# Performance work log

Measured on AMD Instinct MI355X. Metric: run time of the kernel, lower is better.

The kernel has to match this reference:

```python
import jax, jax.numpy as jnp
import numpy as np
import math

B, A, T = 64, 23, 128          # batch, num_agents, max seq len
D, AE, S, H = 256, 32, 6, 8    # d_model, agent_encoding_dim, static_dim, heads
DK = D // H                     # 32
DM = D + AE                     # 288, MHA q/k/v dim
NEG = -1e10                     # masked_fill constant from source


def sinusoidal_pe(pos, d):
    # pos: int array [...], returns [..., d] standard transformer PE at positions pos
    half = jnp.arange(d // 2, dtype=jnp.float32)
    div = jnp.exp(-half * (math.log(10000.0) * 2.0 / d))          # [d/2]
    ang = pos[..., None].astype(jnp.float32) * div                # [..., d/2]
    return jnp.stack([jnp.sin(ang), jnp.cos(ang)], axis=-1).reshape(*pos.shape, d)


def setup_inputs() -> dict:
    key = jax.random.key(0)
    ks = jax.random.split(key, 20)
    std = 0.02
    data = jax.random.normal(ks[0], (B, A, T), jnp.float32)
    lengths = jax.random.randint(ks[1], (B, A), 0, T + 1).astype(jnp.int32)   # mask arg = lengths
    t = jnp.arange(T, dtype=jnp.int32)
    time = jnp.where(t[None, None, :] < lengths[:, :, None], t[None, None, :], -1)  # [B,A,T], -1 = pad
    static = jax.random.normal(ks[2], (B, S), jnp.float32)
    # per-agent Linear(1, D): weight [A, D], bias [A, D]
    W_embed = std * jax.random.normal(ks[3], (A, D), jnp.float32)
    b_embed = std * jax.random.normal(ks[4], (A, D), jnp.float32)
    E_var = std * jax.random.normal(ks[5], (A, AE), jnp.float32)            # VariateEncoding table
    W_static = std * jax.random.normal(ks[6], (S, D), jnp.float32)
    b_static = jnp.zeros((D,), jnp.float32)
    Wq = std * jax.random.normal(ks[7], (DM, D), jnp.float32); bq = jnp.zeros((D,), jnp.float32)
    Wk = std * jax.random.normal(ks[8], (DM, D), jnp.float32); bk = jnp.zeros((D,), jnp.float32)
    Wv = std * jax.random.normal(ks[9], (DM, D), jnp.float32); bv = jnp.zeros((D,), jnp.float32)
    Wo = std * jax.random.normal(ks[10], (D, DM), jnp.float32); bo = jnp.zeros((DM,), jnp.float32)
    Wg = std * jax.random.normal(ks[11], (DM + D, 1), jnp.float32); bg = jnp.zeros((1,), jnp.float32)
    return dict(data=data, time=time, mask=lengths, static=static,
                W_embed=W_embed, b_embed=b_embed, E_var=E_var,
                W_static=W_static, b_static=b_static,
                Wq=Wq, bq=bq, Wk=Wk, bk=bk, Wv=Wv, bv=bv, Wo=Wo, bo=bo,
                Wg=Wg, bg=bg)


def reference(data, time, mask, static, W_embed, b_embed, E_var, W_static, b_static,
              Wq, bq, Wk, bk, Wv, bv, Wo, bo, Wg, bg):
    lengths = mask                                            # [B,A] sequence lengths
    t = jnp.arange(T)
    valid = t[None, None, :] < lengths[:, :, None]            # [B,A,T] bool
    # mask_matrix[i,:len,:len]=1 double loop -> vectorized outer product
    mask4 = valid[:, :, :, None] & valid[:, :, None, :]       # [B,A,T,T]

    # per-agent Linear(1, D) loop -> batched rank-1 affine, then ReLU
    data_embeds = jax.nn.relu(data[..., None] * W_embed[None, :, None, :]
                              + b_embed[None, :, None, :])    # [B,A,T,D]

    # src_pe: sinusoidal positional encoding at (clamped) time values
    pe = sinusoidal_pe(jnp.maximum(time, 0), D)               # [B,A,T,D]
    src = data_embeds + pe

    # variate (agent-id) embedding concat -> [B,A,T,D+AE]; encoder = identity
    var = jnp.broadcast_to(E_var[None, :, None, :], (B, A, T, AE))
    memory = jnp.concatenate([src, var], axis=-1)             # [B,A,T,DM]

    # time-masked mean pool over T
    time_mask = time >= 0                                     # [B,A,T]
    memory = jnp.where(time_mask[..., None], memory, 0.0)
    counts = time_mask.sum(axis=2).astype(memory.dtype)       # [B,A]
    agentwise = memory.sum(axis=2) / (counts[..., None] + 1e-9)  # [B,A,DM]

    # custom MHA (dim='Time'): q_len = 1 per agent, keys/values over T
    q = jnp.einsum('bae,ed->bad', agentwise, Wq) + bq          # [B,A,D]
    k = jnp.einsum('bate,ed->batd', memory, Wk) + bk           # [B,A,T,D]
    v = jnp.einsum('bate,ed->batd', memory, Wv) + bv
    qh = q.reshape(B, A, H, DK)                                # [B,A,H,DK] (q_len=1 squeezed)
    kh = k.reshape(B, A, T, H, DK).transpose(0, 1, 3, 2, 4)    # [B,A,H,T,DK]
    vh = v.reshape(B, A, T, H, DK).transpose(0, 1, 3, 2, 4)
    scores = jnp.einsum('bahd,bahtd->baht', qh, kh) / math.sqrt(DK)  # [B,A,H,T]
    amask = mask4[:, :, 0, :]                                  # [B,A,T] row 0 of per-agent mask
    scores = jnp.where(amask[:, :, None, :], scores, NEG)
    p = jax.nn.softmax(scores, axis=-1)                        # dropout = eval (identity)
    ctx = jnp.einsum('baht,bahtd->bahd', p, vh).reshape(B, A, D)
    agent_feat = jnp.einsum('bad,de->bae', ctx, Wo) + bo       # [B,A,DM]

    # agent-masked mean pool over agents
    agent_mask = counts > 0                                    # [B,A]
    agent_feat = jnp.where(agent_mask[..., None], agent_feat, 0.0)
    denom = agent_mask.sum(axis=1).astype(agent_feat.dtype) + 1e-9
    aggre = agent_feat.sum(axis=1) / denom[:, None]            # [B,DM]

    static_feat = static @ W_static + b_static                 # [B,D]
    all_feature = jnp.concatenate([aggre, static_feat], axis=-1)  # [B,DM+D]
    return all_feature @ Wg + bg                               # [B,1]


if __name__ == '__main__':
    out = reference(**setup_inputs())
    print(out.shape, jnp.asarray(out).dtype)
```

## Files before the change

### kernel.cpp

```cpp
#include <hip/hip_runtime.h>
#include <math.h>

#define NB 64
#define NA 23
#define NT 128
#define ND 256
#define NAE 32
#define NS 6
#define NH 8
#define NDM 288

#define OFF_PET    0
#define OFF_PECUM  32768
#define OFF_WKT    65792
#define OFF_VWO    131328
#define OFF_CST    133632
#define OFF_S      133648

__global__ __launch_bounds__(256) void setup_kernel(
    const float* __restrict__ Wk, const float* __restrict__ Wv,
    const float* __restrict__ Wo, const float* __restrict__ Wg,
    const float* __restrict__ bv, const float* __restrict__ bo,
    const float* __restrict__ W_static, const float* __restrict__ b_static,
    const float* __restrict__ bg, float* __restrict__ ws)
{
    const int blk = blockIdx.x;
    const int tid = threadIdx.x;
    float* peT   = ws + OFF_PET;
    float* PEcum = ws + OFF_PECUM;
    float* WkT   = ws + OFF_WKT;
    float* VWo   = ws + OFF_VWO;
    float* cst   = ws + OFF_CST;

    if (blk < 128) {
        const int g = tid >> 7, t = tid & 127;
        const int e = blk * 2 + g;
        const int i = e >> 1;
        const float kdiv = 0.07195578415606394f;
        const float dv = expf(-(float)i * kdiv);
        const float ang = (float)t * dv;
        const float v = (e & 1) ? cosf(ang) : sinf(ang);
        peT[e * NT + t] = v;
        __shared__ float buf[256];
        buf[tid] = v;
        #pragma unroll
        for (int s = 1; s < 128; s <<= 1) {
            __syncthreads();
            float add = (t >= s) ? buf[tid - s] : 0.f;
            __syncthreads();
            buf[tid] += add;
        }
        __syncthreads();
        PEcum[(t + 1) * ND + e] = buf[tid];
    } else if (blk < 384) {
        const int j = blk - 128;
        const float scale = 0.17677669529663687f;
        WkT[j * 256 + tid] = Wk[tid * ND + j] * scale;
    } else if (blk < 392) {
        const int h = blk - 384;
        __shared__ float wog[32];
        {
            const int jj = tid >> 3, sub = tid & 7;
            const int j = h * 32 + jj;
            float acc = 0.f;
            const int m0 = sub * 36;
            #pragma unroll 4
            for (int m = m0; m < m0 + 36; ++m)
                acc = fmaf(Wo[j * NDM + m], Wg[m], acc);
            acc += __shfl_down(acc, 4, 8);
            acc += __shfl_down(acc, 2, 8);
            acc += __shfl_down(acc, 1, 8);
            if (sub == 0) wog[jj] = acc;
        }
        __syncthreads();
        for (int e = tid; e < NDM; e += 256) {
            float acc = 0.f;
            #pragma unroll 8
            for (int jj = 0; jj < 32; ++jj)
                acc = fmaf(Wv[e * ND + h * 32 + jj], wog[jj], acc);
            VWo[h * NDM + e] = acc;
        }
        if (tid == 0) {
            float acc = 0.f;
            #pragma unroll 8
            for (int jj = 0; jj < 32; ++jj)
                acc = fmaf(bv[h * 32 + jj], wog[jj], acc);
            cst[8 + h] = acc;
        }
    } else {
        const int i = tid >> 5, sub = tid & 31;
        float acc = 0.f;
        if (i < 6) {
            for (int m = sub; m < 256; m += 32)
                acc = fmaf(W_static[i * ND + m], Wg[NDM + m], acc);
        } else if (i == 6) {
            for (int m = sub; m < 256; m += 32)
                acc = fmaf(b_static[m], Wg[NDM + m], acc);
        } else {
            for (int m = sub; m < NDM; m += 32)
                acc = fmaf(bo[m], Wg[m], acc);
        }
        #pragma unroll
        for (int off = 16; off > 0; off >>= 1)
            acc += __shfl_down(acc, off, 32);
        if (sub == 0) cst[i] = (i == 6) ? acc + bg[0] : acc;
    }
}

__global__ __launch_bounds__(256) void main_kernel(
    const float* __restrict__ data, const int* __restrict__ lengths,
    const float* __restrict__ W_embed, const float* __restrict__ b_embed,
    const float* __restrict__ E_var,
    const float* __restrict__ Wq, const float* __restrict__ bq,
    float* __restrict__ ws)
{
    const int wg = blockIdx.x;
    const int a = wg % NA;
    const int tid = threadIdx.x;
    const int L = lengths[wg];

    if (L == 0) {
        if (tid == 0) ws[OFF_S + wg] = 0.f;
        return;
    }

    __shared__ float xs[NT];
    __shared__ float agentwise[NDM];
    __shared__ float qs[ND];
    __shared__ float2 Wb[ND];
    __shared__ __align__(16) float combo[ND * 16];
    __shared__ float evvS[NH];
    __shared__ float red[4];

    const float* peT   = ws + OFF_PET;
    const float* PEcum = ws + OFF_PECUM;
    const float* WkT   = ws + OFF_WKT;
    const float* VWo   = ws + OFF_VWO;
    const float* cstp  = ws + OFF_CST;

    if (tid < NT) xs[tid] = data[wg * NT + tid];
    __syncthreads();
    {
        const int e = tid;
        const float We = W_embed[a * ND + e];
        const float be = b_embed[a * ND + e];
        Wb[e] = make_float2(We, be);
        float acc = 0.f;
        #pragma unroll 4
        for (int t = 0; t < L; ++t)
            acc += fmaxf(fmaf(xs[t], We, be), 0.f);
        agentwise[e] = (acc + PEcum[L * ND + e]) / (float)L;
    }
    if (tid < NAE) agentwise[ND + tid] = E_var[a * NAE + tid];
    __syncthreads();

    {
        const int j = tid;
        float acc = bq[j];
        #pragma unroll 4
        for (int f = 0; f < NDM; ++f)
            acc = fmaf(agentwise[f], Wq[f * ND + j], acc);
        qs[j] = acc;
    }
    __syncthreads();

    {
        const int h = tid >> 5, eo = tid & 31;
        const float* wr = WkT + (h * 32) * 256;
        for (int eb = 0; eb < 8; ++eb) {
            const int e = eb * 32 + eo;
            float acc = 0.f;
            #pragma unroll 8
            for (int j = 0; j < 32; ++j)
                acc = fmaf(wr[j * 256 + e], qs[h * 32 + j], acc);
            combo[e * 16 + h] = acc;
        }
    }
    for (int idx = tid; idx < NH * ND; idx += 256) {
        const int h = idx >> 8, e = idx & 255;
        combo[e * 16 + 8 + h] = VWo[h * NDM + e];
    }
    {
        const int h = tid >> 5, ee = tid & 31;
        float v = E_var[a * NAE + ee] * VWo[h * NDM + ND + ee];
        v += __shfl_down(v, 16, 32);
        v += __shfl_down(v, 8, 32);
        v += __shfl_down(v, 4, 32);
        v += __shfl_down(v, 2, 32);
        v += __shfl_down(v, 1, 32);
        if (ee == 0) evvS[h] = v;
    }
    __syncthreads();

    {
        const int t = tid & 127;
        const int half = tid >> 7;
        const float xt = xs[t];
        float accS[8], accM[8];
        #pragma unroll
        for (int h = 0; h < 8; ++h) { accS[h] = 0.f; accM[h] = 0.f; }
        const int ebase = half * 128;
        const float4* comboV = (const float4*)combo + ebase * 4;
        const float* peCol = peT + ebase * NT + t;
        #pragma unroll 2
        for (int ee = 0; ee < 128; ++ee) {
            const float2 wb = Wb[ebase + ee];
            const float m = fmaxf(fmaf(xt, wb.x, wb.y), 0.f) + peCol[ee * NT];
            const float4 c0 = comboV[ee * 4 + 0];
            const float4 c1 = comboV[ee * 4 + 1];
            const float4 c2 = comboV[ee * 4 + 2];
            const float4 c3 = comboV[ee * 4 + 3];
            accS[0] = fmaf(m, c0.x, accS[0]);
            accS[1] = fmaf(m, c0.y, accS[1]);
            accS[2] = fmaf(m, c0.z, accS[2]);
            accS[3] = fmaf(m, c0.w, accS[3]);
            accS[4] = fmaf(m, c1.x, accS[4]);
            accS[5] = fmaf(m, c1.y, accS[5]);
            accS[6] = fmaf(m, c1.z, accS[6]);
            accS[7] = fmaf(m, c1.w, accS[7]);
            accM[0] = fmaf(m, c2.x, accM[0]);
            accM[1] = fmaf(m, c2.y, accM[1]);
            accM[2] = fmaf(m, c2.z, accM[2]);
            accM[3] = fmaf(m, c2.w, accM[3]);
            accM[4] = fmaf(m, c3.x, accM[4]);
            accM[5] = fmaf(m, c3.y, accM[5]);
            accM[6] = fmaf(m, c3.z, accM[6]);
            accM[7] = fmaf(m, c3.w, accM[7]);
        }
        __syncthreads();
        float* sc   = combo;
        float* mvb  = combo + 1024;
        float* scP1 = combo + 2048;
        float* mvP1 = combo + 3072;
        if (half == 1) {
            #pragma unroll
            for (int h = 0; h < 8; ++h) {
                scP1[h * NT + t] = accS[h];
                mvP1[h * NT + t] = accM[h];
            }
        }
        __syncthreads();
        if (half == 0) {
            #pragma unroll
            for (int h = 0; h < 8; ++h) {
                sc[h * NT + t]  = accS[h] + scP1[h * NT + t];
                mvb[h * NT + t] = accM[h] + mvP1[h * NT + t];
            }
        }
    }
    __syncthreads();

    {
        const float* sc  = combo;
        const float* mvb = combo + 1024;
        const int wv = tid >> 6, lane = tid & 63;
        float wsum = 0.f;
        for (int hh = 0; hh < 2; ++hh) {
            const int h = wv * 2 + hh;
            float s1 = (lane < L) ? sc[h * NT + lane] : -3e38f;
            float s2 = (lane + 64 < L) ? sc[h * NT + 64 + lane] : -3e38f;
            float mx = fmaxf(s1, s2);
            #pragma unroll
            for (int off = 32; off > 0; off >>= 1)
                mx = fmaxf(mx, __shfl_down(mx, off, 64));
            mx = __shfl(mx, 0, 64);
            const float vbv = evvS[h] + cstp[8 + h];
            float e1 = (lane < L) ? __expf(s1 - mx) : 0.f;
            float e2 = (lane + 64 < L) ? __expf(s2 - mx) : 0.f;
            float num = e1 * (mvb[h * NT + lane] + vbv);
            num = fmaf(e2, mvb[h * NT + 64 + lane] + vbv, num);
            float den = e1 + e2;
            #pragma unroll
            for (int off = 32; off > 0; off >>= 1) {
                num += __shfl_down(num, off, 64);
                den += __shfl_down(den, off, 64);
            }
            if (lane == 0) wsum += num / den;
        }
        if (lane == 0) red[wv] = wsum;
    }
    __syncthreads();
    if (tid == 0) {
        ws[OFF_S + wg] = cstp[7] + red[0] + red[1] + red[2] + red[3];
    }
}

__global__ __launch_bounds__(64) void final_kernel(
    const float* __restrict__ statics, const int* __restrict__ lengths,
    const float* __restrict__ ws, float* __restrict__ out)
{
    const int b = threadIdx.x;
    const float* s_arr = ws + OFF_S;
    const float* cst = ws + OFF_CST;
    float sum = 0.f;
    int n = 0;
    for (int a = 0; a < NA; ++a) {
        if (lengths[b * NA + a] > 0) { sum += s_arr[b * NA + a]; ++n; }
    }
    float o = sum / ((float)n + 1e-9f);
    #pragma unroll
    for (int i = 0; i < NS; ++i)
        o = fmaf(statics[b * NS + i], cst[i], o);
    o += cst[6];
    out[b] = o;
}

extern "C" void kernel_launch(void* const* d_in, const int* in_sizes, int n_in,
                              void* d_out, int out_size, void* d_ws, size_t ws_size,
                              hipStream_t stream) {
    const float* data     = (const float*)d_in[0];
    const int*   mask     = (const int*)d_in[2];
    const float* statics  = (const float*)d_in[3];
    const float* W_embed  = (const float*)d_in[4];
    const float* b_embed  = (const float*)d_in[5];
    const float* E_var    = (const float*)d_in[6];
    const float* W_static = (const float*)d_in[7];
    const float* b_static = (const float*)d_in[8];
    const float* Wq       = (const float*)d_in[9];
    const float* bq       = (const float*)d_in[10];
    const float* Wk       = (const float*)d_in[11];
    const float* Wv       = (const float*)d_in[13];
    const float* bv       = (const float*)d_in[14];
    const float* Wo       = (const float*)d_in[15];
    const float* bo       = (const float*)d_in[16];
    const float* Wg       = (const float*)d_in[17];
    const float* bg       = (const float*)d_in[18];
    float* out = (float*)d_out;
    float* ws  = (float*)d_ws;

    setup_kernel<<<dim3(393), dim3(256), 0, stream>>>(Wk, Wv, Wo, Wg, bv, bo,
                                                      W_static, b_static, bg, ws);
    main_kernel<<<dim3(NB * NA), dim3(256), 0, stream>>>(data, mask, W_embed, b_embed,
                                                         E_var, Wq, bq, ws);
    final_kernel<<<dim3(1), dim3(64), 0, stream>>>(statics, mask, ws, out);
}
```

Baseline: 165.5 us.

## Fuse final reduction into main kernel and adapt score loop to sequence length

Removes the separate final kernel: each block bumps a global atomic counter, and the last block to finish computes the per-batch masked mean and static projection. The main kernel also vectorises the Q projection with float4 Wq loads split over four chunks, uses multiple accumulators in the embedding-sum and K-fold loops, and pads the combo layout to a stride of 20. For sequences of length 64 or less, the score/value loop splits the embedding dimension four ways instead of two, which halves per-thread work. The counter is reset inside the setup kernel, and the fused tail adds atomics and fences in exchange for one fewer launch.

Measured after the change: 214.6 us. 29.7% more time.

```diff
diff --git a/kernel.cpp b/kernel.cpp
--- a/kernel.cpp
+++ b/kernel.cpp
@@ -12,6 +12,7 @@
 
 #define OFF_PET    0
 #define OFF_PECUM  32768
+#define OFF_CNT    32768
 #define OFF_WKT    65792
 #define OFF_VWO    131328
 #define OFF_CST    133632
@@ -88,6 +89,7 @@
             cst[8 + h] = acc;
         }
     } else {
+        if (tid == 0) ws[OFF_CNT] = 0.0f;
         const int i = tid >> 5, sub = tid & 31;
         float acc = 0.f;
         if (i < 6) {
@@ -112,6 +114,7 @@
     const float* __restrict__ W_embed, const float* __restrict__ b_embed,
     const float* __restrict__ E_var,
     const float* __restrict__ Wq, const float* __restrict__ bq,
+    const float* __restrict__ statics, float* __restrict__ out,
     float* __restrict__ ws)
 {
     const int wg = blockIdx.x;
@@ -119,18 +122,14 @@
     const int tid = threadIdx.x;
     const int L = lengths[wg];
 
-    if (L == 0) {
-        if (tid == 0) ws[OFF_S + wg] = 0.f;
-        return;
-    }
-
     __shared__ float xs[NT];
     __shared__ float agentwise[NDM];
     __shared__ float qs[ND];
     __shared__ float2 Wb[ND];
-    __shared__ __align__(16) float combo[ND * 16];
+    __shared__ __align__(16) float combo[ND * 20];
     __shared__ float evvS[NH];
     __shared__ float red[4];
+    __shared__ int lastFlag;
 
     const float* peT   = ws + OFF_PET;
     const float* PEcum = ws + OFF_PECUM;
@@ -138,171 +137,211 @@
     const float* VWo   = ws + OFF_VWO;
     const float* cstp  = ws + OFF_CST;
 
-    if (tid < NT) xs[tid] = data[wg * NT + tid];
-    __syncthreads();
-    {
-        const int e = tid;
-        const float We = W_embed[a * ND + e];
-        const float be = b_embed[a * ND + e];
-        Wb[e] = make_float2(We, be);
-        float acc = 0.f;
-        #pragma unroll 4
-        for (int t = 0; t < L; ++t)
-            acc += fmaxf(fmaf(xs[t], We, be), 0.f);
-        agentwise[e] = (acc + PEcum[L * ND + e]) / (float)L;
+    if (L > 0) {
+        if (tid < NT) xs[tid] = data[wg * NT + tid];
+        __syncthreads();
+        {
+            const int e = tid;
+            const float We = W_embed[a * ND + e];
+            const float be = b_embed[a * ND + e];
+            Wb[e] = make_float2(We, be);
+            float s0 = 0.f, s1 = 0.f, s2 = 0.f, s3 = 0.f;
+            int t = 0;
+            for (; t + 4 <= L; t += 4) {
+                s0 += fmaxf(fmaf(xs[t],     We, be), 0.f);
+                s1 += fmaxf(fmaf(xs[t + 1], We, be), 0.f);
+                s2 += fmaxf(fmaf(xs[t + 2], We, be), 0.f);
+                s3 += fmaxf(fmaf(xs[t + 3], We, be), 0.f);
+            }
+            for (; t < L; ++t)
+                s0 += fmaxf(fmaf(xs[t], We, be), 0.f);
+            agentwise[e] = (((s0 + s1) + (s2 + s3)) + PEcum[L * ND + e]) / (float)L;
+        }
+        if (tid < NAE) agentwise[ND + tid] = E_var[a * NAE + tid];
+        __syncthreads();
+
+        {
+            const int lane = tid & 63;
+            const int fc = tid >> 6;
+            const float4* Wq4 = (const float4*)Wq;
+            float a0 = 0.f, a1 = 0.f, a2 = 0.f, a3 = 0.f;
+            const int f0 = fc * 72;
+            #pragma unroll 4
+            for (int f = f0; f < f0 + 72; ++f) {
+                const float ag = agentwise[f];
+                const float4 w = Wq4[f * 64 + lane];
+                a0 = fmaf(ag, w.x, a0);
+                a1 = fmaf(ag, w.y, a1);
+                a2 = fmaf(ag, w.z, a2);
+                a3 = fmaf(ag, w.w, a3);
+            }
+            ((float4*)combo)[fc * 64 + lane] = make_float4(a0, a1, a2, a3);
+        }
+        __syncthreads();
+        qs[tid] = bq[tid] + combo[tid] + combo[256 + tid] + combo[512 + tid] + combo[768 + tid];
+        __syncthreads();
+
+        {
+            const int h = tid >> 5, eo = tid & 31;
+            const float* wr = WkT + (h * 32) * 256;
+            const float* qh = qs + h * 32;
+            for (int eb = 0; eb < 8; ++eb) {
+                const int e = eb * 32 + eo;
+                float acc = 0.f, acc2 = 0.f;
+                #pragma unroll
+                for (int j = 0; j < 32; j += 2) {
+                    acc  = fmaf(wr[ j      * 256 + e], qh[j],     acc);
+                    acc2 = fmaf(wr[(j + 1) * 256 + e], qh[j + 1], acc2);
+                }
+                combo[e * 20 + h] = acc + acc2;
+            }
+        }
+        for (int idx = tid; idx < NH * ND; idx += 256) {
+            const int h = idx >> 8, e = idx & 255;
+            combo[e * 20 + 8 + h] = VWo[h * NDM + e];
+        }
+        {
+            const int h = tid >> 5, ee = tid & 31;
+            float v = agentwise[ND + ee] * VWo[h * NDM + ND + ee];
+            v += __shfl_down(v, 16, 32);
+            v += __shfl_down(v, 8, 32);
+            v += __shfl_down(v, 4, 32);
+            v += __shfl_down(v, 2, 32);
+            v += __shfl_down(v, 1, 32);
+            if (ee == 0) evvS[h] = v;
+        }
+        __syncthreads();
+
+        {
+            const int shift = (L > 64) ? 7 : 6;
+            const int Tpad  = 1 << shift;
+            const int P     = 256 >> shift;
+            const int t     = tid & (Tpad - 1);
+            const int c     = tid >> shift;
+            const int ebase = c * Tpad;
+            const float xt = xs[t];
+            float accS[8], accM[8];
+            #pragma unroll
+            for (int h = 0; h < 8; ++h) { accS[h] = 0.f; accM[h] = 0.f; }
+            const float4* comboV = (const float4*)combo;
+            const float* peCol = peT + ebase * NT + t;
+            #pragma unroll 2
+            for (int ee = 0; ee < Tpad; ++ee) {
+                const int e = ebase + ee;
+                const float2 wb = Wb[e];
+                const float m = fmaxf(fmaf(xt, wb.x, wb.y), 0.f) + peCol[ee * NT];
+                const float4 c0 = comboV[e * 5 + 0];
+                const float4 c1 = comboV[e * 5 + 1];
+                const float4 c2 = comboV[e * 5 + 2];
+                const float4 c3 = comboV[e * 5 + 3];
+                accS[0] = fmaf(m, c0.x, accS[0]);
+                accS[1] = fmaf(m, c0.y, accS[1]);
+                accS[2] = fmaf(m, c0.z, accS[2]);
+                accS[3] = fmaf(m, c0.w, accS[3]);
+                accS[4] = fmaf(m, c1.x, accS[4]);
+                accS[5] = fmaf(m, c1.y, accS[5]);
+                accS[6] = fmaf(m, c1.z, accS[6]);
+                accS[7] = fmaf(m, c1.w, accS[7]);
+                accM[0] = fmaf(m, c2.x, accM[0]);
+                accM[1] = fmaf(m, c2.y, accM[1]);
+                accM[2] = fmaf(m, c2.z, accM[2]);
+                accM[3] = fmaf(m, c2.w, accM[3]);
+                accM[4] = fmaf(m, c3.x, accM[4]);
+                accM[5] = fmaf(m, c3.y, accM[5]);
+                accM[6] = fmaf(m, c3.z, accM[6]);
+                accM[7] = fmaf(m, c3.w, accM[7]);
+            }
+            __syncthreads();
+            float* sc  = combo;
+            float* mvb = combo + 1024;
+            float* sp  = combo + 2048;
+            float* mp  = sp + (P - 1) * 8 * Tpad;
+            if (c > 0) {
+                float* spc = sp + (c - 1) * 8 * Tpad;
+                float* mpc = mp + (c - 1) * 8 * Tpad;
+                #pragma unroll
+                for (int h = 0; h < 8; ++h) {
+                    spc[h * Tpad + t] = accS[h];
+                    mpc[h * Tpad + t] = accM[h];
+                }
+            }
+            __syncthreads();
+            if (c == 0) {
+                #pragma unroll
+                for (int h = 0; h < 8; ++h) {
+                    float s = accS[h], m = accM[h];
+                    for (int cc = 0; cc < P - 1; ++cc) {
+                        s += sp[cc * 8 * Tpad + h * Tpad + t];
+                        m += mp[cc * 8 * Tpad + h * Tpad + t];
+                    }
+                    sc[h * NT + t]  = s;
+                    mvb[h * NT + t] = m;
+                }
+            }
+        }
+        __syncthreads();
+
+        {
+            const float* sc  = combo;
+            const float* mvb = combo + 1024;
+            const int wv = tid >> 6, lane = tid & 63;
+            float wsum = 0.f;
+            for (int hh = 0; hh < 2; ++hh) {
+                const int h = wv * 2 + hh;
+                float s1 = (lane < L) ? sc[h * NT + lane] : -3e38f;
+                float s2 = (lane + 64 < L) ? sc[h * NT + 64 + lane] : -3e38f;
+                float mx = fmaxf(s1, s2);
+                #pragma unroll
+                for (int off = 32; off > 0; off >>= 1)
+                    mx = fmaxf(mx, __shfl_down(mx, off, 64));
+                mx = __shfl(mx, 0, 64);
+                const float vbv = evvS[h] + cstp[8 + h];
+                float e1 = (lane < L) ? __expf(s1 - mx) : 0.f;
+                float e2 = (lane + 64 < L) ? __expf(s2 - mx) : 0.f;
+                float num = e1 * (mvb[h * NT + lane] + vbv);
+                num = fmaf(e2, mvb[h * NT + 64 + lane] + vbv, num);
+                float den = e1 + e2;
+                #pragma unroll
+                for (int off = 32; off > 0; off >>= 1) {
+                    num += __shfl_down(num, off, 64);
+                    den += __shfl_down(den, off, 64);
+                }
+                if (lane == 0) wsum += num / den;
+            }
+            if (lane == 0) red[wv] = wsum;
+        }
+        __syncthreads();
+        if (tid == 0)
+            ws[OFF_S + wg] = cstp[7] + red[0] + red[1] + red[2] + red[3];
+    } else {
+        if (tid == 0) ws[OFF_S + wg] = 0.f;
     }
-    if (tid < NAE) agentwise[ND + tid] = E_var[a * NAE + tid];
-    __syncthreads();
-
-    {
-        const int j = tid;
-        float acc = bq[j];
-        #pragma unroll 4
-        for (int f = 0; f < NDM; ++f)
-            acc = fmaf(agentwise[f], Wq[f * ND + j], acc);
-        qs[j] = acc;
+
+    if (tid == 0) {
+        __threadfence();
+        const int prev = atomicAdd((int*)(ws + OFF_CNT), 1);
+        lastFlag = (prev == NB * NA - 1) ? 1 : 0;
     }
     __syncthreads();
-
-    {
-        const int h = tid >> 5, eo = tid & 31;
-        const float* wr = WkT + (h * 32) * 256;
-        for (int eb = 0; eb < 8; ++eb) {
-            const int e = eb * 32 + eo;
-            float acc = 0.f;
-            #pragma unroll 8
-            for (int j = 0; j < 32; ++j)
-                acc = fmaf(wr[j * 256 + e], qs[h * 32 + j], acc);
-            combo[e * 16 + h] = acc;
-        }
+    if (lastFlag && tid < NB) {
+        __threadfence();
+        const int b = tid;
+        float* s_arr = ws + OFF_S;
+        float sum = 0.f;
+        int n = 0;
+        for (int aa = 0; aa < NA; ++aa) {
+            if (lengths[b * NA + aa] > 0) {
+                sum += atomicAdd(s_arr + b * NA + aa, 0.f);
+                ++n;
+            }
+        }
+        float o = sum / ((float)n + 1e-9f);
+        #pragma unroll
+        for (int i = 0; i < NS; ++i)
+            o = fmaf(statics[b * NS + i], cstp[i], o);
+        o += cstp[6];
+        out[b] = o;
     }
-    for (int idx = tid; idx < NH * ND; idx += 256) {
-        const int h = idx >> 8, e = idx & 255;
-        combo[e * 16 + 8 + h] = VWo[h * NDM + e];
-    }
-    {
-        const int h = tid >> 5, ee = tid & 31;
-        float v = E_var[a * NAE + ee] * VWo[h * NDM + ND + ee];
-        v += __shfl_down(v, 16, 32);
-        v += __shfl_down(v, 8, 32);
-        v += __shfl_down(v, 4, 32);
-        v += __shfl_down(v, 2, 32);
-        v += __shfl_down(v, 1, 32);
-        if (ee == 0) evvS[h] = v;
-    }
-    __syncthreads();
-
-    {
-        const int t = tid & 127;
-        const int half = tid >> 7;
-        const float xt = xs[t];
-        float accS[8], accM[8];
-        #pragma unroll
-        for (int h = 0; h < 8; ++h) { accS[h] = 0.f; accM[h] = 0.f; }
-        const int ebase = half * 128;
-        const float4* comboV = (const float4*)combo + ebase * 4;
-        const float* peCol = peT + ebase * NT + t;
-        #pragma unroll 2
-        for (int ee = 0; ee < 128; ++ee) {
-            const float2 wb = Wb[ebase + ee];
-            const float m = fmaxf(fmaf(xt, wb.x, wb.y), 0.f) + peCol[ee * NT];
-            const float4 c0 = comboV[ee * 4 + 0];
-            const float4 c1 = comboV[ee * 4 + 1];
-            const float4 c2 = comboV[ee * 4 + 2];
-            const float4 c3 = comboV[ee * 4 + 3];
-            accS[0] = fmaf(m, c0.x, accS[0]);
-            accS[1] = fmaf(m, c0.y, accS[1]);
-            accS[2] = fmaf(m, c0.z, accS[2]);
-            accS[3] = fmaf(m, c0.w, accS[3]);
-            accS[4] = fmaf(m, c1.x, accS[4]);
-            accS[5] = fmaf(m, c1.y, accS[5]);
-            accS[6] = fmaf(m, c1.z, accS[6]);
-            accS[7] = fmaf(m, c1.w, accS[7]);
-            accM[0] = fmaf(m, c2.x, accM[0]);
-            accM[1] = fmaf(m, c2.y, accM[1]);
-            accM[2] = fmaf(m, c2.z, accM[2]);
-            accM[3] = fmaf(m, c2.w, accM[3]);
-            accM[4] = fmaf(m, c3.x, accM[4]);
-            accM[5] = fmaf(m, c3.y, accM[5]);
-            accM[6] = fmaf(m, c3.z, accM[6]);
-            accM[7] = fmaf(m, c3.w, accM[7]);
-        }
-        __syncthreads();
-        float* sc   = combo;
-        float* mvb  = combo + 1024;
-        float* scP1 = combo + 2048;
-        float* mvP1 = combo + 3072;
-        if (half == 1) {
-            #pragma unroll
-            for (int h = 0; h < 8; ++h) {
-                scP1[h * NT + t] = accS[h];
-                mvP1[h * NT + t] = accM[h];
-            }
-        }
-        __syncthreads();
-        if (half == 0) {
-            #pragma unroll
-            for (int h = 0; h < 8; ++h) {
-                sc[h * NT + t]  = accS[h] + scP1[h * NT + t];
-                mvb[h * NT + t] = accM[h] + mvP1[h * NT + t];
-            }
-        }
-    }
-    __syncthreads();
-
-    {
-        const float* sc  = combo;
-        const float* mvb = combo + 1024;
-        const int wv = tid >> 6, lane = tid & 63;
-        float wsum = 0.f;
-        for (int hh = 0; hh < 2; ++hh) {
-            const int h = wv * 2 + hh;
-            float s1 = (lane < L) ? sc[h * NT + lane] : -3e38f;
-            float s2 = (lane + 64 < L) ? sc[h * NT + 64 + lane] : -3e38f;
-            float mx = fmaxf(s1, s2);
-            #pragma unroll
-            for (int off = 32; off > 0; off >>= 1)
-                mx = fmaxf(mx, __shfl_down(mx, off, 64));
-            mx = __shfl(mx, 0, 64);
-            const float vbv = evvS[h] + cstp[8 + h];
-            float e1 = (lane < L) ? __expf(s1 - mx) : 0.f;
-            float e2 = (lane + 64 < L) ? __expf(s2 - mx) : 0.f;
-            float num = e1 * (mvb[h * NT + lane] + vbv);
-            num = fmaf(e2, mvb[h * NT + 64 + lane] + vbv, num);
-            float den = e1 + e2;
-            #pragma unroll
-            for (int off = 32; off > 0; off >>= 1) {
-                num += __shfl_down(num, off, 64);
-                den += __shfl_down(den, off, 64);
-            }
-            if (lane == 0) wsum += num / den;
-        }
-        if (lane == 0) red[wv] = wsum;
-    }
-    __syncthreads();
-    if (tid == 0) {
-        ws[OFF_S + wg] = cstp[7] + red[0] + red[1] + red[2] + red[3];
-    }
-}
-
-__global__ __launch_bounds__(64) void final_kernel(
-    const float* __restrict__ statics, const int* __restrict__ lengths,
-    const float* __restrict__ ws, float* __restrict__ out)
-{
-    const int b = threadIdx.x;
-    const float* s_arr = ws + OFF_S;
-    const float* cst = ws + OFF_CST;
-    float sum = 0.f;
-    int n = 0;
-    for (int a = 0; a < NA; ++a) {
-        if (lengths[b * NA + a] > 0) { sum += s_arr[b * NA + a]; ++n; }
-    }
-    float o = sum / ((float)n + 1e-9f);
-    #pragma unroll
-    for (int i = 0; i < NS; ++i)
-        o = fmaf(statics[b * NS + i], cst[i], o);
-    o += cst[6];
-    out[b] = o;
 }
 
 extern "C" void kernel_launch(void* const* d_in, const int* in_sizes, int n_in,
@@ -331,6 +370,5 @@
     setup_kernel<<<dim3(393), dim3(256), 0, stream>>>(Wk, Wv, Wo, Wg, bv, bo,
                                                       W_static, b_static, bg, ws);
     main_kernel<<<dim3(NB * NA), dim3(256), 0, stream>>>(data, mask, W_embed, b_embed,
-                                                         E_var, Wq, bq, ws);
-    final_kernel<<<dim3(1), dim3(64), 0, stream>>>(statics, mask, ws, out);
+                                                         E_var, Wq, bq, statics, out, ws);
 }
```

## Restructure main kernel projections, swizzle combo layout, add short-sequence path

Applied to the files above, without the earlier changes.

The setup kernel now copies Wk scaled in its original layout with float4 loads instead of transposing it. In the main kernel, the q projection is split across four waves that each read float4 Wq rows, with the partial sums combined through shared memory. The K-fold becomes a per-thread dot product over contiguous Wk rows, and combo rows are XOR-swizzled to cut LDS bank conflicts. The embedding and PE inner loop gets multiple accumulators and PE prefetching, and a separate path for L<=64 splits the feature dimension four ways so that no threads sit idle on padded timesteps. The cost is more code, extra shared-memory reductions and a larger register footprint.

New measurement: 192.4 us. 1.16x slower.

```diff
diff --git a/kernel.cpp b/kernel.cpp
--- a/kernel.cpp
+++ b/kernel.cpp
@@ -12,7 +12,7 @@
 
 #define OFF_PET    0
 #define OFF_PECUM  32768
-#define OFF_WKT    65792
+#define OFF_WKS    65792
 #define OFF_VWO    131328
 #define OFF_CST    133632
 #define OFF_S      133648
@@ -28,7 +28,6 @@
     const int tid = threadIdx.x;
     float* peT   = ws + OFF_PET;
     float* PEcum = ws + OFF_PECUM;
-    float* WkT   = ws + OFF_WKT;
     float* VWo   = ws + OFF_VWO;
     float* cst   = ws + OFF_CST;
 
@@ -52,12 +51,14 @@
         }
         __syncthreads();
         PEcum[(t + 1) * ND + e] = buf[tid];
-    } else if (blk < 384) {
-        const int j = blk - 128;
+    } else if (blk < 192) {
         const float scale = 0.17677669529663687f;
-        WkT[j * 256 + tid] = Wk[tid * ND + j] * scale;
-    } else if (blk < 392) {
-        const int h = blk - 384;
+        const int i = (blk - 128) * 256 + tid;
+        const float4 w = ((const float4*)Wk)[i];
+        ((float4*)(ws + OFF_WKS))[i] = make_float4(w.x * scale, w.y * scale,
+                                                   w.z * scale, w.w * scale);
+    } else if (blk < 200) {
+        const int h = blk - 192;
         __shared__ float wog[32];
         {
             const int jj = tid >> 3, sub = tid & 7;
@@ -107,6 +108,38 @@
     }
 }
 
+#define EBODY(EE, RR) do {                                                   \
+    const int e_ = ebase + (EE);                                             \
+    const float2 wb = Wb[e_];                                                \
+    const float m = fmaxf(fmaf(xt, wb.x, wb.y), 0.f) + pcur[RR];             \
+    const float4 c0 = comboV[e_ * 4 + (0 ^ (RR))];                           \
+    const float4 c1 = comboV[e_ * 4 + (1 ^ (RR))];                           \
+    const float4 c2 = comboV[e_ * 4 + (2 ^ (RR))];                           \
+    const float4 c3 = comboV[e_ * 4 + (3 ^ (RR))];                           \
+    accS[0] = fmaf(m, c0.x, accS[0]); accS[1] = fmaf(m, c0.y, accS[1]);      \
+    accS[2] = fmaf(m, c0.z, accS[2]); accS[3] = fmaf(m, c0.w, accS[3]);      \
+    accS[4] = fmaf(m, c1.x, accS[4]); accS[5] = fmaf(m, c1.y, accS[5]);      \
+    accS[6] = fmaf(m, c1.z, accS[6]); accS[7] = fmaf(m, c1.w, accS[7]);      \
+    accM[0] = fmaf(m, c2.x, accM[0]); accM[1] = fmaf(m, c2.y, accM[1]);      \
+    accM[2] = fmaf(m, c2.z, accM[2]); accM[3] = fmaf(m, c2.w, accM[3]);      \
+    accM[4] = fmaf(m, c3.x, accM[4]); accM[5] = fmaf(m, c3.y, accM[5]);      \
+    accM[6] = fmaf(m, c3.z, accM[6]); accM[7] = fmaf(m, c3.w, accM[7]);      \
+} while (0)
+
+#define E_LOOP(TPC)                                                          \
+    pcur[0] = peCol[0 * NT]; pcur[1] = peCol[1 * NT];                        \
+    pcur[2] = peCol[2 * NT]; pcur[3] = peCol[3 * NT];                        \
+    _Pragma("unroll 2")                                                      \
+    for (int ee = 0; ee < (TPC); ee += 4) {                                  \
+        const float pn0 = peCol[(ee + 4) * NT];                              \
+        const float pn1 = peCol[(ee + 5) * NT];                              \
+        const float pn2 = peCol[(ee + 6) * NT];                              \
+        const float pn3 = peCol[(ee + 7) * NT];                              \
+        EBODY(ee + 0, 0); EBODY(ee + 1, 1);                                  \
+        EBODY(ee + 2, 2); EBODY(ee + 3, 3);                                  \
+        pcur[0] = pn0; pcur[1] = pn1; pcur[2] = pn2; pcur[3] = pn3;          \
+    }
+
 __global__ __launch_bounds__(256) void main_kernel(
     const float* __restrict__ data, const int* __restrict__ lengths,
     const float* __restrict__ W_embed, const float* __restrict__ b_embed,
@@ -126,7 +159,7 @@
 
     __shared__ float xs[NT];
     __shared__ float agentwise[NDM];
-    __shared__ float qs[ND];
+    __shared__ __align__(16) float qs[ND];
     __shared__ float2 Wb[ND];
     __shared__ __align__(16) float combo[ND * 16];
     __shared__ float evvS[NH];
@@ -134,7 +167,7 @@
 
     const float* peT   = ws + OFF_PET;
     const float* PEcum = ws + OFF_PECUM;
-    const float* WkT   = ws + OFF_WKT;
+    const float* WkS   = ws + OFF_WKS;
     const float* VWo   = ws + OFF_VWO;
     const float* cstp  = ws + OFF_CST;
 
@@ -145,44 +178,74 @@
         const float We = W_embed[a * ND + e];
         const float be = b_embed[a * ND + e];
         Wb[e] = make_float2(We, be);
-        float acc = 0.f;
+        float s0 = 0.f, s1 = 0.f, s2 = 0.f, s3 = 0.f;
+        int t = 0;
+        for (; t + 4 <= L; t += 4) {
+            s0 += fmaxf(fmaf(xs[t],     We, be), 0.f);
+            s1 += fmaxf(fmaf(xs[t + 1], We, be), 0.f);
+            s2 += fmaxf(fmaf(xs[t + 2], We, be), 0.f);
+            s3 += fmaxf(fmaf(xs[t + 3], We, be), 0.f);
+        }
+        for (; t < L; ++t)
+            s0 += fmaxf(fmaf(xs[t], We, be), 0.f);
+        agentwise[e] = (((s0 + s1) + (s2 + s3)) + PEcum[L * ND + e]) / (float)L;
+    }
+    if (tid < NAE) agentwise[ND + tid] = E_var[a * NAE + tid];
+    __syncthreads();
+
+    {
+        const int lane = tid & 63;
+        const int fc = tid >> 6;
+        const float4* Wq4 = (const float4*)Wq;
+        float a0 = 0.f, a1 = 0.f, a2 = 0.f, a3 = 0.f;
+        const int f0 = fc * 72;
         #pragma unroll 4
-        for (int t = 0; t < L; ++t)
-            acc += fmaxf(fmaf(xs[t], We, be), 0.f);
-        agentwise[e] = (acc + PEcum[L * ND + e]) / (float)L;
-    }
-    if (tid < NAE) agentwise[ND + tid] = E_var[a * NAE + tid];
+        for (int f = f0; f < f0 + 72; ++f) {
+            const float ag = agentwise[f];
+            const float4 w = Wq4[f * 64 + lane];
+            a0 = fmaf(ag, w.x, a0);
+            a1 = fmaf(ag, w.y, a1);
+            a2 = fmaf(ag, w.z, a2);
+            a3 = fmaf(ag, w.w, a3);
+        }
+        ((float4*)combo)[fc * 64 + lane] = make_float4(a0, a1, a2, a3);
+    }
+    __syncthreads();
+    qs[tid] = bq[tid] + combo[tid] + combo[256 + tid] + combo[512 + tid] + combo[768 + tid];
     __syncthreads();
 
     {
-        const int j = tid;
-        float acc = bq[j];
-        #pragma unroll 4
-        for (int f = 0; f < NDM; ++f)
-            acc = fmaf(agentwise[f], Wq[f * ND + j], acc);
-        qs[j] = acc;
-    }
-    __syncthreads();
-
-    {
-        const int h = tid >> 5, eo = tid & 31;
-        const float* wr = WkT + (h * 32) * 256;
-        for (int eb = 0; eb < 8; ++eb) {
-            const int e = eb * 32 + eo;
-            float acc = 0.f;
-            #pragma unroll 8
-            for (int j = 0; j < 32; ++j)
-                acc = fmaf(wr[j * 256 + e], qs[h * 32 + j], acc);
-            combo[e * 16 + h] = acc;
-        }
-    }
-    for (int idx = tid; idx < NH * ND; idx += 256) {
-        const int h = idx >> 8, e = idx & 255;
-        combo[e * 16 + 8 + h] = VWo[h * NDM + e];
+        const int e = tid;
+        const float4* wrow = (const float4*)(WkS + e * 256);
+        const float4* qs4  = (const float4*)qs;
+        float qk[8];
+        #pragma unroll
+        for (int h = 0; h < 8; ++h) {
+            float a0 = 0.f, a1 = 0.f, a2 = 0.f, a3 = 0.f;
+            #pragma unroll
+            for (int jq = 0; jq < 8; ++jq) {
+                const float4 w = wrow[h * 8 + jq];
+                const float4 q = qs4[h * 8 + jq];
+                a0 = fmaf(w.x, q.x, a0);
+                a1 = fmaf(w.y, q.y, a1);
+                a2 = fmaf(w.z, q.z, a2);
+                a3 = fmaf(w.w, q.w, a3);
+            }
+            qk[h] = (a0 + a1) + (a2 + a3);
+        }
+        float vwo[8];
+        #pragma unroll
+        for (int h = 0; h < 8; ++h) vwo[h] = VWo[h * NDM + e];
+        const int r = e & 3;
+        float4* row = (float4*)combo + e * 4;
+        row[0 ^ r] = make_float4(qk[0], qk[1], qk[2], qk[3]);
+        row[1 ^ r] = make_float4(qk[4], qk[5], qk[6], qk[7]);
+        row[2 ^ r] = make_float4(vwo[0], vwo[1], vwo[2], vwo[3]);
+        row[3 ^ r] = make_float4(vwo[4], vwo[5], vwo[6], vwo[7]);
     }
     {
         const int h = tid >> 5, ee = tid & 31;
-        float v = E_var[a * NAE + ee] * VWo[h * NDM + ND + ee];
+        float v = agentwise[ND + ee] * VWo[h * NDM + ND + ee];
         v += __shfl_down(v, 16, 32);
         v += __shfl_down(v, 8, 32);
         v += __shfl_down(v, 4, 32);
@@ -192,41 +255,17 @@
     }
     __syncthreads();
 
-    {
-        const int t = tid & 127;
-        const int half = tid >> 7;
+    const float4* comboV = (const float4*)combo;
+    if (L > 64) {
+        const int t = tid & 127, half = tid >> 7;
+        const int ebase = half * 128;
         const float xt = xs[t];
+        const float* peCol = peT + ebase * NT + t;
+        float pcur[4];
         float accS[8], accM[8];
         #pragma unroll
         for (int h = 0; h < 8; ++h) { accS[h] = 0.f; accM[h] = 0.f; }
-        const int ebase = half * 128;
-        const float4* comboV = (const float4*)combo + ebase * 4;
-        const float* peCol = peT + ebase * NT + t;
-        #pragma unroll 2
-        for (int ee = 0; ee < 128; ++ee) {
-            const float2 wb = Wb[ebase + ee];
-            const float m = fmaxf(fmaf(xt, wb.x, wb.y), 0.f) + peCol[ee * NT];
-            const float4 c0 = comboV[ee * 4 + 0];
-            const float4 c1 = comboV[ee * 4 + 1];
-            const float4 c2 = comboV[ee * 4 + 2];
-            const float4 c3 = comboV[ee * 4 + 3];
-            accS[0] = fmaf(m, c0.x, accS[0]);
-            accS[1] = fmaf(m, c0.y, accS[1]);
-            accS[2] = fmaf(m, c0.z, accS[2]);
-            accS[3] = fmaf(m, c0.w, accS[3]);
-            accS[4] = fmaf(m, c1.x, accS[4]);
-            accS[5] = fmaf(m, c1.y, accS[5]);
-            accS[6] = fmaf(m, c1.z, accS[6]);
-            accS[7] = fmaf(m, c1.w, accS[7]);
-            accM[0] = fmaf(m, c2.x, accM[0]);
-            accM[1] = fmaf(m, c2.y, accM[1]);
-            accM[2] = fmaf(m, c2.z, accM[2]);
-            accM[3] = fmaf(m, c2.w, accM[3]);
-            accM[4] = fmaf(m, c3.x, accM[4]);
-            accM[5] = fmaf(m, c3.y, accM[5]);
-            accM[6] = fmaf(m, c3.z, accM[6]);
-            accM[7] = fmaf(m, c3.w, accM[7]);
-        }
+        E_LOOP(128);
         __syncthreads();
         float* sc   = combo;
         float* mvb  = combo + 1024;
@@ -247,42 +286,97 @@
                 mvb[h * NT + t] = accM[h] + mvP1[h * NT + t];
             }
         }
-    }
-    __syncthreads();
-
-    {
-        const float* sc  = combo;
-        const float* mvb = combo + 1024;
-        const int wv = tid >> 6, lane = tid & 63;
-        float wsum = 0.f;
-        for (int hh = 0; hh < 2; ++hh) {
-            const int h = wv * 2 + hh;
-            float s1 = (lane < L) ? sc[h * NT + lane] : -3e38f;
-            float s2 = (lane + 64 < L) ? sc[h * NT + 64 + lane] : -3e38f;
-            float mx = fmaxf(s1, s2);
+        __syncthreads();
+        {
+            const int wv = tid >> 6, lane = tid & 63;
+            float wsum = 0.f;
+            for (int hh = 0; hh < 2; ++hh) {
+                const int h = wv * 2 + hh;
+                float s1 = (lane < L) ? sc[h * NT + lane] : -3e38f;
+                float s2 = (lane + 64 < L) ? sc[h * NT + 64 + lane] : -3e38f;
+                float mx = fmaxf(s1, s2);
+                #pragma unroll
+                for (int off = 32; off > 0; off >>= 1)
+                    mx = fmaxf(mx, __shfl_down(mx, off, 64));
+                mx = __shfl(mx, 0, 64);
+                const float vbv = evvS[h] + cstp[8 + h];
+                float e1 = (lane < L) ? __expf(s1 - mx) : 0.f;
+                float e2 = (lane + 64 < L) ? __expf(s2 - mx) : 0.f;
+                float num = e1 * (mvb[h * NT + lane] + vbv);
+                num = fmaf(e2, mvb[h * NT + 64 + lane] + vbv, num);
+                float den = e1 + e2;
+                #pragma unroll
+                for (int off = 32; off > 0; off >>= 1) {
+                    num += __shfl_down(num, off, 64);
+                    den += __shfl_down(den, off, 64);
+                }
+                if (lane == 0) wsum += num / den;
+            }
+            if (lane == 0) red[wv] = wsum;
+        }
+    } else {
+        const int t = tid & 63, c = tid >> 6;
+        const int ebase = c * 64;
+        const float xt = xs[t];
+        const float* peCol = peT + ebase * NT + t;
+        float pcur[4];
+        float accS[8], accM[8];
+        #pragma unroll
+        for (int h = 0; h < 8; ++h) { accS[h] = 0.f; accM[h] = 0.f; }
+        E_LOOP(64);
+        __syncthreads();
+        float* sc  = combo;
+        float* mvb = combo + 512;
+        float* sp  = combo + 1024;
+        if (c > 0) {
+            float* bse = sp + (c - 1) * 1024;
             #pragma unroll
-            for (int off = 32; off > 0; off >>= 1)
-                mx = fmaxf(mx, __shfl_down(mx, off, 64));
-            mx = __shfl(mx, 0, 64);
-            const float vbv = evvS[h] + cstp[8 + h];
-            float e1 = (lane < L) ? __expf(s1 - mx) : 0.f;
-            float e2 = (lane + 64 < L) ? __expf(s2 - mx) : 0.f;
-            float num = e1 * (mvb[h * NT + lane] + vbv);
-            num = fmaf(e2, mvb[h * NT + 64 + lane] + vbv, num);
-            float den = e1 + e2;
+            for (int h = 0; h < 8; ++h) {
+                bse[h * 64 + t]       = accS[h];
+                bse[512 + h * 64 + t] = accM[h];
+            }
+        }
+        __syncthreads();
+        if (c == 0) {
             #pragma unroll
-            for (int off = 32; off > 0; off >>= 1) {
-                num += __shfl_down(num, off, 64);
-                den += __shfl_down(den, off, 64);
-            }
-            if (lane == 0) wsum += num / den;
-        }
-        if (lane == 0) red[wv] = wsum;
-    }
-    __syncthreads();
-    if (tid == 0) {
+            for (int h = 0; h < 8; ++h) {
+                float s = accS[h] + sp[h * 64 + t] + sp[1024 + h * 64 + t]
+                                  + sp[2048 + h * 64 + t];
+                float m = accM[h] + sp[512 + h * 64 + t] + sp[1536 + h * 64 + t]
+                                  + sp[2560 + h * 64 + t];
+                sc[h * 64 + t]  = s;
+                mvb[h * 64 + t] = m;
+            }
+        }
+        __syncthreads();
+        {
+            const int wv = tid >> 6, lane = tid & 63;
+            float wsum = 0.f;
+            for (int hh = 0; hh < 2; ++hh) {
+                const int h = wv * 2 + hh;
+                float s1 = (lane < L) ? sc[h * 64 + lane] : -3e38f;
+                float mx = s1;
+                #pragma unroll
+                for (int off = 32; off > 0; off >>= 1)
+                    mx = fmaxf(mx, __shfl_down(mx, off, 64));
+                mx = __shfl(mx, 0, 64);
+                const float vbv = evvS[h] + cstp[8 + h];
+                float e1 = (lane < L) ? __expf(s1 - mx) : 0.f;
+                float num = e1 * (mvb[h * 64 + lane] + vbv);
+                float den = e1;
+                #pragma unroll
+                for (int off = 32; off > 0; off >>= 1) {
+                    num += __shfl_down(num, off, 64);
+                    den += __shfl_down(den, off, 64);
+                }
+                if (lane == 0) wsum += num / den;
+            }
+            if (lane == 0) red[wv] = wsum;
+        }
+    }
+    __syncthreads();
+    if (tid == 0)
         ws[OFF_S + wg] = cstp[7] + red[0] + red[1] + red[2] + red[3];
-    }
 }
 
 __global__ __launch_bounds__(64) void final_kernel(
@@ -328,7 +422,7 @@
     float* out = (float*)d_out;
     float* ws  = (float*)d_ws;
 
-    setup_kernel<<<dim3(393), dim3(256), 0, stream>>>(Wk, Wv, Wo, Wg, bv, bo,
+    setup_kernel<<<dim3(201), dim3(256), 0, stream>>>(Wk, Wv, Wo, Wg, bv, bo,
                                                       W_static, b_static, bg, ws);
     main_kernel<<<dim3(NB * NA), dim3(256), 0, stream>>>(data, mask, W_embed, b_embed,
                                                          E_var, Wq, bq, ws);
```
